# Optimization experiments

Hardware: AMD Instinct MI355X
Metric: run time of the kernel (lower is better)

## Reference

```python
import jax, jax.numpy as jnp
import numpy as np

T = 4096          # total packed tokens (4 docs x 1024)
NUM_DOCS = 4
H = 16            # n_heads
D = 64            # head_dim == v_head_dim
TOPK = 64         # per-token top-k KV selection (<= min doc len)


def setup_inputs() -> dict:
    key = jax.random.key(0)
    kq, kk, kv, ki, ks = jax.random.split(key, 5)
    q = jax.random.normal(kq, (T, H, D), dtype=jnp.float32)
    k = jax.random.normal(kk, (T, H, D), dtype=jnp.float32)
    v = jax.random.normal(kv, (T, H, D), dtype=jnp.float32)
    # 4 equal-length documents of 1024 tokens
    cu_seqlens = (jnp.arange(NUM_DOCS + 1, dtype=jnp.int32) * (T // NUM_DOCS))
    # global top-k indices; reference clamps them into the owning document
    topk_indices = jax.random.randint(ki, (T, TOPK), 0, T, dtype=jnp.int32)
    # selector scores in (0,1), like indexer softmax outputs
    topk_scores = jax.random.uniform(ks, (T, TOPK), dtype=jnp.float32)
    return {
        "q_packed": q,
        "k_packed": k,
        "v_packed": v,
        "cu_seqlens": cu_seqlens,
        "topk_indices": topk_indices,
        "topk_scores": topk_scores,
    }


def reference(q_packed, k_packed, v_packed, cu_seqlens, topk_indices, topk_scores):
    total_tokens, n_heads, head_dim = q_packed.shape
    scale = head_dim ** -0.5

    # Per-token document assignment (vectorized replacement for the doc loop).
    tok = jnp.arange(total_tokens, dtype=cu_seqlens.dtype)
    seg = jnp.searchsorted(cu_seqlens[1:], tok, side="right")  # (T,) doc id
    start = cu_seqlens[seg]                                    # (T,)
    seq_len = cu_seqlens[seg + 1] - start                      # (T,)

    # Localize and clamp top-k indices into the owning document, then
    # convert back to global packed indices for gathering.
    local = jnp.clip(topk_indices - start[:, None], 0, (seq_len - 1)[:, None])
    gidx = start[:, None] + local                              # (T, K)

    k_gathered = k_packed[gidx]   # (T, K, H, D)
    v_gathered = v_packed[gidx]   # (T, K, H, D)

    # q . k_sel, softmax over the k selected keys
    scores = jnp.einsum("thd,tkhd->thk", q_packed, k_gathered) * scale
    w = jax.nn.softmax(scores, axis=-1)                        # (T, H, K)

    # Modulate by selector scores (head-shared) and renormalize.
    w = w * topk_scores[:, None, :]
    w = w / (jnp.sum(w, axis=-1, keepdims=True) + 1e-12)

    out = jnp.einsum("thk,tkhd->thd", w, v_gathered)           # (T, H, D)
    return out
```

## Files before the change

kernel.cpp:

```cpp
#include <hip/hip_runtime.h>
#include <hip/hip_fp16.h>


#define T_TOK 4096
#define NH    16
#define HD    64
#define KSEL  64
#define KV_ELEMS (T_TOK * NH * HD)

typedef _Float16 h2v __attribute__((ext_vector_type(2)));

static __device__ __forceinline__ h2v u2h2v(unsigned u) {
    return __builtin_bit_cast(h2v, u);
}
static __device__ __forceinline__ __half2 u2h2(unsigned u) {
    return __builtin_bit_cast(__half2, u);
}
static __device__ __forceinline__ unsigned h22u(__half2 h) {
    return __builtin_bit_cast(unsigned, h);
}
static __device__ __forceinline__ h2v f2h2v(float a, float b) {
    __half2 t = __floats2half2_rn(a, b);
    return __builtin_bit_cast(h2v, t);
}

__global__ __launch_bounds__(256) void cvt_fp16(
    const float4* __restrict__ kM, const float4* __restrict__ vM,
    uint2* __restrict__ kH, uint2* __restrict__ vH)
{
    const int n4 = KV_ELEMS / 4;
    const int i  = blockIdx.x * blockDim.x + threadIdx.x;
    const bool isK = i < n4;
    const float4 f = isK ? kM[i] : vM[i - n4];
    __half2 lo = __floats2half2_rn(f.x, f.y);
    __half2 hi = __floats2half2_rn(f.z, f.w);
    uint2 u;
    u.x = h22u(lo);
    u.y = h22u(hi);
    if (isK) kH[i] = u; else vH[i - n4] = u;
}

__global__ __launch_bounds__(256) void dsa_sparse_attn(
    const float*  __restrict__ qM,
    const __half* __restrict__ kH,
    const __half* __restrict__ vH,
    const int*    __restrict__ cu,
    const int*    __restrict__ tidx,
    const float*  __restrict__ tsc,
    float*        __restrict__ out,
    int num_docs)
{
    const int wave = threadIdx.x >> 6;
    const int lane = threadIdx.x & 63;

    const int b            = blockIdx.x;
    const int xcd          = b & 7;
    const int j            = b >> 3;
    const int token_block  = j & 255;
    const int slice_within = j >> 8;
    const int s            = xcd + (slice_within << 3);
    const int h            = s & (NH - 1);
    const int t            = (s >> 4) * (T_TOK / 4) + token_block * 4 + wave;
    const int gid          = t * NH + h;

    int seg = 0;
    for (int i = 1; i < num_docs; ++i)
        if (t >= cu[i]) seg = i;
    const int start = cu[seg];
    const int len   = cu[seg + 1] - start;

    int idx = tidx[t * KSEL + lane];
    int loc = idx - start;
    loc = loc < 0 ? 0 : loc;
    loc = loc > len - 1 ? len - 1 : loc;
    const int g = start + loc;
    const float sc = tsc[t * KSEL + lane];

    const int laneCol = lane & 3;
    const int laneRow = lane >> 2;
    const int laneQ8  = lane >> 3;
    const int laneC8  = lane & 7;

    const uint4* kf = (const uint4*)kH;
    const uint4* vf = (const uint4*)vH;
    const int hc1 = h * 8 + laneCol;
    const int hc3 = h * 8 + laneC8;

    const float4* qv = (const float4*)(qM + gid * HD);
    const float4 f0 = qv[laneCol * 2];
    const float4 f1 = qv[laneCol * 2 + 1];
    const float4 f2 = qv[8 + laneCol * 2];
    const float4 f3 = qv[8 + laneCol * 2 + 1];
    h2v qa[4] = { f2h2v(f0.x, f0.y), f2h2v(f0.z, f0.w),
                  f2h2v(f1.x, f1.y), f2h2v(f1.z, f1.w) };
    h2v qb[4] = { f2h2v(f2.x, f2.y), f2h2v(f2.z, f2.w),
                  f2h2v(f3.x, f3.y), f2h2v(f3.z, f3.w) };

    float score = 0.f;
    #pragma unroll
    for (int rg = 0; rg < 4; ++rg) {
        const int grow = __shfl(g, rg * 16 + laneRow, 64);
        const uint4 kA = kf[grow * 128 + hc1];
        const uint4 kB = kf[grow * 128 + hc1 + 4];
        float p = 0.f;
        p = __builtin_amdgcn_fdot2(u2h2v(kA.x), qa[0], p, false);
        p = __builtin_amdgcn_fdot2(u2h2v(kA.y), qa[1], p, false);
        p = __builtin_amdgcn_fdot2(u2h2v(kA.z), qa[2], p, false);
        p = __builtin_amdgcn_fdot2(u2h2v(kA.w), qa[3], p, false);
        p = __builtin_amdgcn_fdot2(u2h2v(kB.x), qb[0], p, false);
        p = __builtin_amdgcn_fdot2(u2h2v(kB.y), qb[1], p, false);
        p = __builtin_amdgcn_fdot2(u2h2v(kB.z), qb[2], p, false);
        p = __builtin_amdgcn_fdot2(u2h2v(kB.w), qb[3], p, false);
        p += __shfl_xor(p, 1, 64);
        p += __shfl_xor(p, 2, 64);
        const float got = __shfl(p, (lane & 15) << 2, 64);
        if (rg == (lane >> 4)) score = got;
    }
    score *= 0.125f;

    uint4 vreg[8];
    {
        const int r0 = __shfl(g, 0 * 8 + laneQ8, 64);
        const int r1 = __shfl(g, 1 * 8 + laneQ8, 64);
        const int r2 = __shfl(g, 2 * 8 + laneQ8, 64);
        const int r3 = __shfl(g, 3 * 8 + laneQ8, 64);
        const int r4 = __shfl(g, 4 * 8 + laneQ8, 64);
        const int r5 = __shfl(g, 5 * 8 + laneQ8, 64);
        const int r6 = __shfl(g, 6 * 8 + laneQ8, 64);
        const int r7 = __shfl(g, 7 * 8 + laneQ8, 64);
        vreg[0] = vf[r0 * 128 + hc3];
        vreg[1] = vf[r1 * 128 + hc3];
        vreg[2] = vf[r2 * 128 + hc3];
        vreg[3] = vf[r3 * 128 + hc3];
        vreg[4] = vf[r4 * 128 + hc3];
        vreg[5] = vf[r5 * 128 + hc3];
        vreg[6] = vf[r6 * 128 + hc3];
        vreg[7] = vf[r7 * 128 + hc3];
    }

    const float e = __expf(score);
    const float p = e * sc;
    float S2 = p;
    #pragma unroll
    for (int off = 32; off; off >>= 1)
        S2 += __shfl_xor(S2, off, 64);
    const float w = p / S2;

    const unsigned hb  = (unsigned)__builtin_bit_cast(unsigned short, __float2half(w));
    const unsigned wpk = hb | (hb << 16);

    __half2 acc[4];
    acc[0] = u2h2(0u); acc[1] = u2h2(0u); acc[2] = u2h2(0u); acc[3] = u2h2(0u);
    #pragma unroll
    for (int i = 0; i < 8; ++i) {
        const unsigned wu = (unsigned)__shfl((int)wpk, i * 8 + laneQ8, 64);
        const __half2 wk2 = u2h2(wu);
        acc[0] = __hfma2(wk2, u2h2(vreg[i].x), acc[0]);
        acc[1] = __hfma2(wk2, u2h2(vreg[i].y), acc[1]);
        acc[2] = __hfma2(wk2, u2h2(vreg[i].z), acc[2]);
        acc[3] = __hfma2(wk2, u2h2(vreg[i].w), acc[3]);
    }
    #pragma unroll
    for (int off = 8; off <= 32; off <<= 1) {
        #pragma unroll
        for (int jj = 0; jj < 4; ++jj) {
            const unsigned o = (unsigned)__shfl_xor((int)h22u(acc[jj]), off, 64);
            acc[jj] = __hadd2(acc[jj], u2h2(o));
        }
    }
    if (laneQ8 == 0) {
        const float2 a0 = __half22float2(acc[0]);
        const float2 a1 = __half22float2(acc[1]);
        const float2 a2 = __half22float2(acc[2]);
        const float2 a3 = __half22float2(acc[3]);
        float4* op = (float4*)(out + gid * HD + laneC8 * 8);
        op[0] = make_float4(a0.x, a0.y, a1.x, a1.y);
        op[1] = make_float4(a2.x, a2.y, a3.x, a3.y);
    }
}

extern "C" void kernel_launch(void* const* d_in, const int* in_sizes, int n_in,
                              void* d_out, int out_size, void* d_ws, size_t ws_size,
                              hipStream_t stream) {
    const float* q   = (const float*)d_in[0];
    const float* k   = (const float*)d_in[1];
    const float* v   = (const float*)d_in[2];
    const int*   cu  = (const int*)d_in[3];
    const int*   ti  = (const int*)d_in[4];
    const float* ts  = (const float*)d_in[5];
    float*       out = (float*)d_out;
    const int num_docs = in_sizes[3] - 1;

    __half* kH = (__half*)d_ws;
    __half* vH = kH + KV_ELEMS;

    const int n4 = KV_ELEMS / 4;
    hipLaunchKernelGGL(cvt_fp16, dim3(2 * n4 / 256), dim3(256), 0, stream,
                       (const float4*)k, (const float4*)v,
                       (uint2*)kH, (uint2*)vH);

    const int total_waves = T_TOK * NH;
    hipLaunchKernelGGL(dsa_sparse_attn, dim3(total_waves / 4), dim3(256), 0,
                       stream, q, (const __half*)kH, (const __half*)vH,
                       cu, ti, ts, out, num_docs);
}
```

Before: 147.6 us.

## Gather V rows into LDS via async global_load_lds and defer normalization

```diff
diff --git a/kernel.cpp b/kernel.cpp
--- a/kernel.cpp
+++ b/kernel.cpp
@@ -50,6 +50,8 @@
     float*        __restrict__ out,
     int num_docs)
 {
+    __shared__ uint4 sV[4][512];
+
     const int wave = threadIdx.x >> 6;
     const int lane = threadIdx.x & 63;
 
@@ -82,9 +84,20 @@
     const int laneC8  = lane & 7;
 
     const uint4* kf = (const uint4*)kH;
-    const uint4* vf = (const uint4*)vH;
     const int hc1 = h * 8 + laneCol;
-    const int hc3 = h * 8 + laneC8;
+
+    {
+        const __half* vbase = vH;
+        #pragma unroll
+        for (int i = 0; i < 8; ++i) {
+            const int gr = __shfl(g, i * 8 + laneQ8, 64);
+            const __half* gp = vbase + ((gr * NH + h) << 6) + (laneC8 << 3);
+            __builtin_amdgcn_global_load_lds(
+                (const __attribute__((address_space(1))) unsigned int*)gp,
+                (__attribute__((address_space(3))) unsigned int*)&sV[wave][i * 64],
+                16, 0, 0);
+        }
+    }
 
     const float4* qv = (const float4*)(qM + gid * HD);
     const float4 f0 = qv[laneCol * 2];
@@ -118,48 +131,30 @@
     }
     score *= 0.125f;
 
-    uint4 vreg[8];
-    {
-        const int r0 = __shfl(g, 0 * 8 + laneQ8, 64);
-        const int r1 = __shfl(g, 1 * 8 + laneQ8, 64);
-        const int r2 = __shfl(g, 2 * 8 + laneQ8, 64);
-        const int r3 = __shfl(g, 3 * 8 + laneQ8, 64);
-        const int r4 = __shfl(g, 4 * 8 + laneQ8, 64);
-        const int r5 = __shfl(g, 5 * 8 + laneQ8, 64);
-        const int r6 = __shfl(g, 6 * 8 + laneQ8, 64);
-        const int r7 = __shfl(g, 7 * 8 + laneQ8, 64);
-        vreg[0] = vf[r0 * 128 + hc3];
-        vreg[1] = vf[r1 * 128 + hc3];
-        vreg[2] = vf[r2 * 128 + hc3];
-        vreg[3] = vf[r3 * 128 + hc3];
-        vreg[4] = vf[r4 * 128 + hc3];
-        vreg[5] = vf[r5 * 128 + hc3];
-        vreg[6] = vf[r6 * 128 + hc3];
-        vreg[7] = vf[r7 * 128 + hc3];
-    }
-
     const float e = __expf(score);
     const float p = e * sc;
+    const unsigned hb  = (unsigned)__builtin_bit_cast(unsigned short, __float2half(p));
+    const unsigned ppk = hb | (hb << 16);
+
+    asm volatile("s_waitcnt vmcnt(0)" ::: "memory");
+    __half2 acc[4];
+    acc[0] = u2h2(0u); acc[1] = u2h2(0u); acc[2] = u2h2(0u); acc[3] = u2h2(0u);
+    #pragma unroll
+    for (int i = 0; i < 8; ++i) {
+        const unsigned pu = (unsigned)__shfl((int)ppk, i * 8 + laneQ8, 64);
+        const __half2 pk2 = u2h2(pu);
+        const uint4 vv = sV[wave][i * 64 + lane];
+        acc[0] = __hfma2(pk2, u2h2(vv.x), acc[0]);
+        acc[1] = __hfma2(pk2, u2h2(vv.y), acc[1]);
+        acc[2] = __hfma2(pk2, u2h2(vv.z), acc[2]);
+        acc[3] = __hfma2(pk2, u2h2(vv.w), acc[3]);
+    }
+
     float S2 = p;
     #pragma unroll
     for (int off = 32; off; off >>= 1)
         S2 += __shfl_xor(S2, off, 64);
-    const float w = p / S2;
-
-    const unsigned hb  = (unsigned)__builtin_bit_cast(unsigned short, __float2half(w));
-    const unsigned wpk = hb | (hb << 16);
-
-    __half2 acc[4];
-    acc[0] = u2h2(0u); acc[1] = u2h2(0u); acc[2] = u2h2(0u); acc[3] = u2h2(0u);
-    #pragma unroll
-    for (int i = 0; i < 8; ++i) {
-        const unsigned wu = (unsigned)__shfl((int)wpk, i * 8 + laneQ8, 64);
-        const __half2 wk2 = u2h2(wu);
-        acc[0] = __hfma2(wk2, u2h2(vreg[i].x), acc[0]);
-        acc[1] = __hfma2(wk2, u2h2(vreg[i].y), acc[1]);
-        acc[2] = __hfma2(wk2, u2h2(vreg[i].z), acc[2]);
-        acc[3] = __hfma2(wk2, u2h2(vreg[i].w), acc[3]);
-    }
+
     #pragma unroll
     for (int off = 8; off <= 32; off <<= 1) {
         #pragma unroll
@@ -168,14 +163,16 @@
             acc[jj] = __hadd2(acc[jj], u2h2(o));
         }
     }
+
     if (laneQ8 == 0) {
+        const float inv = __builtin_amdgcn_rcpf(S2);
         const float2 a0 = __half22float2(acc[0]);
         const float2 a1 = __half22float2(acc[1]);
         const float2 a2 = __half22float2(acc[2]);
         const float2 a3 = __half22float2(acc[3]);
         float4* op = (float4*)(out + gid * HD + laneC8 * 8);
-        op[0] = make_float4(a0.x, a0.y, a1.x, a1.y);
-        op[1] = make_float4(a2.x, a2.y, a3.x, a3.y);
+        op[0] = make_float4(a0.x * inv, a0.y * inv, a1.x * inv, a1.y * inv);
+        op[1] = make_float4(a2.x * inv, a2.y * inv, a3.x * inv, a3.y * inv);
     }
 }
 
```

Measured after the change: 155.3 us. 1.05x slower.
